# Optimization experiments

Hardware: AMD Instinct MI355X
Metric: run time of the kernel (lower is better)

## Reference

```python
import jax, jax.numpy as jnp
import numpy as np

N = 512      # state dim n
K = 8        # num_regimes
H = 256      # hidden dim for g0/g1/gate MLPs
B = 8192     # batch
INIT_SCALE = 0.1


def _mlp(x, w1, b1, w2, b2, w3, b3):
    # 2 hidden SiLU layers + linear head (matches ScalarMLP/GateNet with num_layers=2)
    h = jax.nn.silu(x @ w1 + b1)
    h = jax.nn.silu(h @ w2 + b2)
    return h @ w3 + b3


def setup_inputs() -> dict:
    key = jax.random.key(0)
    ks = jax.random.split(key, 12)

    def lin(k, fi, fo):
        kw, kb = jax.random.split(k)
        s = 1.0 / np.sqrt(fi)  # torch nn.Linear default init range
        w = jax.random.uniform(kw, (fi, fo), minval=-s, maxval=s, dtype=jnp.float32)
        b = jax.random.uniform(kb, (fo,), minval=-s, maxval=s, dtype=jnp.float32)
        return w, b

    g0_w1, g0_b1 = lin(ks[0], N, H)
    g0_w2, g0_b2 = lin(ks[1], H, H)
    g0_w3, g0_b3 = lin(ks[2], H, 1)
    g1_w1, g1_b1 = lin(ks[3], N, H)
    g1_w2, g1_b2 = lin(ks[4], H, H)
    g1_w3, g1_b3 = lin(ks[5], H, 1)
    gt_w1, gt_b1 = lin(ks[6], N, H)
    gt_w2, gt_b2 = lin(ks[7], H, H)
    gt_w3, gt_b3 = lin(ks[8], H, K)
    W = jax.random.uniform(ks[9], (K, N, N), minval=-INIT_SCALE, maxval=INIT_SCALE, dtype=jnp.float32)
    z = jax.random.normal(ks[10], (B, 2 * N), dtype=jnp.float32)
    return dict(z=z,
                g0_w1=g0_w1, g0_b1=g0_b1, g0_w2=g0_w2, g0_b2=g0_b2, g0_w3=g0_w3, g0_b3=g0_b3,
                g1_w1=g1_w1, g1_b1=g1_b1, g1_w2=g1_w2, g1_b2=g1_b2, g1_w3=g1_w3, g1_b3=g1_b3,
                gt_w1=gt_w1, gt_b1=gt_b1, gt_w2=gt_w2, gt_b2=gt_b2, gt_w3=gt_w3, gt_b3=gt_b3,
                W=W)


def reference(z,
              g0_w1, g0_b1, g0_w2, g0_b2, g0_w3, g0_b3,
              g1_w1, g1_b1, g1_w2, g1_b2, g1_w3, g1_b3,
              gt_w1, gt_b1, gt_w2, gt_b2, gt_w3, gt_b3,
              W):
    n = W.shape[-1]
    x0, x1 = z[:, :n], z[:, n:]

    def U(x0_, x1_):
        e0 = jnp.sum(_mlp(x0_, g0_w1, g0_b1, g0_w2, g0_b2, g0_w3, g0_b3))  # scalar
        e1 = jnp.sum(_mlp(x1_, g1_w1, g1_b1, g1_w2, g1_b2, g1_w3, g1_b3))
        alpha = jax.nn.softmax(_mlp(x0_, gt_w1, gt_b1, gt_w2, gt_b2, gt_w3, gt_b3), axis=-1)  # [B,K]
        # per-sample per-regime bilinear x1^T W_k x0 -> avoids materializing [B,n,n] W_eff
        q = jnp.einsum('bi,kij,bj->bk', x1_, W, x0_)
        return e0 + e1 + jnp.sum(alpha * q)

    grad_x0, grad_x1 = jax.grad(U, argnums=(0, 1))(x0, x1)
    return jnp.concatenate([-grad_x0, -grad_x1], axis=-1)  # [B, 2n]
```

## Files before the change

### kernel.cpp

```cpp
#include <hip/hip_runtime.h>
#include <cstdint>
#include <cstddef>

constexpr int BTOT = 8192, N = 512, H = 256, K = 8;

typedef __attribute__((ext_vector_type(8))) short short8v;
typedef __attribute__((ext_vector_type(4))) float f32x4;

__device__ __forceinline__ float bf2f(unsigned short u) {
    return __uint_as_float(((uint32_t)u) << 16);
}
__device__ __forceinline__ unsigned short f2bf(float f) {
    uint32_t u = __float_as_uint(f);
    uint32_t r = (u + 0x7FFFu + ((u >> 16) & 1u)) >> 16;
    return (unsigned short)r;
}

typedef __attribute__((address_space(3))) unsigned int lds_uint;
typedef __attribute__((address_space(1))) const unsigned int glob_uint;
__device__ __forceinline__ void async16(const unsigned short* g, unsigned short* l) {
    __builtin_amdgcn_global_load_lds((glob_uint*)g, (lds_uint*)l, 16, 0, 0);
}

struct GArg {
    const unsigned short* A;
    const unsigned short* Bt;
    const float* bias;
    const unsigned short* dmul;
    unsigned short* ob;
    unsigned short* ob2;
    float* of;
    int lda, ldbt, Ka, lddm, ldob, ldof;
};
struct GPack { GArg g[5]; };

enum { EPI_BF = 0, EPI_FWD = 1, EPI_BWD2 = 2, EPI_NEG = 3, EPI_NEGW = 4 };

template<int EPI>
__device__ __forceinline__ void gemm_body(const GArg& g, int m0, int n0,
                                          unsigned short* As, unsigned short* Bs)
{
    const int tid = threadIdx.x;
    const int lane = tid & 63, wave = tid >> 6;
    const int wr = (wave >> 1) * 64, wc = (wave & 1) * 64;
    const int rr = lane & 15;
    const int kb = ((lane >> 4) ^ (lane & 3)) << 3;

    const int r0 = tid >> 2;
    const int ko0 = (((tid & 3) ^ (r0 & 3)) << 3);
    const unsigned short* gA0 = g.A + (size_t)(m0 + r0) * g.lda + ko0;
    const unsigned short* gA1 = g.A + (size_t)(m0 + r0 + 64) * g.lda + ko0;
    const unsigned short* gB0 = g.Bt + (size_t)(n0 + r0) * g.ldbt + ko0;
    const unsigned short* gB1 = g.Bt + (size_t)(n0 + r0 + 64) * g.ldbt + ko0;

    auto stage = [&](int t, int buf) {
        const int k0 = t << 5;
        async16(gA0 + k0, As + buf * 4096 + tid * 8);
        async16(gA1 + k0, As + buf * 4096 + (tid + 256) * 8);
        async16(gB0 + k0, Bs + buf * 4096 + tid * 8);
        async16(gB1 + k0, Bs + buf * 4096 + (tid + 256) * 8);
    };

    f32x4 acc[4][4];
    #pragma unroll
    for (int i = 0; i < 4; ++i)
        #pragma unroll
        for (int j = 0; j < 4; ++j) acc[i][j] = (f32x4){0.f, 0.f, 0.f, 0.f};

    const int nt = g.Ka >> 5;

    stage(0, 0);
    if (nt > 1) stage(1, 1);

    int buf = 0;
    for (int t = 0; t < nt; ++t) {
        if (t + 1 < nt) { asm volatile("s_waitcnt vmcnt(4)" ::: "memory"); }
        else            { asm volatile("s_waitcnt vmcnt(0)" ::: "memory"); }
        __builtin_amdgcn_s_barrier();
        if (t + 2 < nt) {
            int b2 = buf + 2; if (b2 >= 3) b2 -= 3;
            stage(t + 2, b2);
        }
        short8v af[4], bfr[4];
        #pragma unroll
        for (int i = 0; i < 4; ++i)
            af[i] = *(const short8v*)(As + buf * 4096 + (wr + i * 16 + rr) * 32 + kb);
        #pragma unroll
        for (int j = 0; j < 4; ++j)
            bfr[j] = *(const short8v*)(Bs + buf * 4096 + (wc + j * 16 + rr) * 32 + kb);
        #pragma unroll
        for (int i = 0; i < 4; ++i)
            #pragma unroll
            for (int j = 0; j < 4; ++j)
                acc[i][j] = __builtin_amdgcn_mfma_f32_16x16x32_bf16(af[i], bfr[j], acc[i][j], 0, 0, 0);
        if (++buf == 3) buf = 0;
    }

    const int orow = (lane >> 4) * 4;
    #pragma unroll
    for (int i = 0; i < 4; ++i) {
        #pragma unroll
        for (int e = 0; e < 4; ++e) {
            const int row = m0 + wr + i * 16 + orow + e;
            #pragma unroll
            for (int j = 0; j < 4; ++j) {
                const int col = n0 + wc + rr + j * 16;
                float v = acc[i][j][e];
                if constexpr (EPI == EPI_BF) {
                    g.ob[(size_t)row * g.ldob + col] = f2bf(v);
                } else if constexpr (EPI == EPI_FWD) {
                    float p = v + g.bias[col];
                    float s = 1.f / (1.f + expf(-p));
                    if (g.ob) g.ob[(size_t)row * g.ldob + col] = f2bf(p * s);
                    g.ob2[(size_t)row * g.ldob + col] = f2bf(s * (1.f + p * (1.f - s)));
                } else if constexpr (EPI == EPI_BWD2) {
                    float t = v * bf2f(g.dmul[(size_t)row * g.lddm + col]);
                    g.ob[(size_t)row * g.ldob + col] = f2bf(t);
                } else if constexpr (EPI == EPI_NEG) {
                    g.of[(size_t)row * g.ldof + col] -= v;
                } else {
                    g.of[(size_t)row * g.ldof + col] = -v;
                }
            }
        }
    }
}

template<int EPI>
__global__ __launch_bounds__(256) void gemm_g(GArg ga0, GArg ga1, GArg ga2)
{
    __shared__ __attribute__((aligned(16))) unsigned short As[3 * 128 * 32];
    __shared__ __attribute__((aligned(16))) unsigned short Bs[3 * 128 * 32];
    const int z = blockIdx.z;
    const GArg g = (z == 0) ? ga0 : (z == 1) ? ga1 : ga2;
    gemm_body<EPI>(g, blockIdx.y * 128, blockIdx.x * 128, As, Bs);
}

__global__ __launch_bounds__(256) void gemm_l1bil(GPack P)
{
    __shared__ __attribute__((aligned(16))) unsigned short As[3 * 128 * 32];
    __shared__ __attribute__((aligned(16))) unsigned short Bs[3 * 128 * 32];
    const int xb = blockIdx.x;
    if (xb < 32) {
        gemm_body<EPI_BF>(P.g[blockIdx.z], blockIdx.y * 128, xb * 128, As, Bs);
    } else {
        gemm_body<EPI_FWD>(P.g[2 + (xb - 32)], blockIdx.y * 128, blockIdx.z * 128, As, Bs);
    }
}

__global__ __launch_bounds__(256) void k_cvt_z(const float* __restrict__ z,
                                               unsigned short* __restrict__ o) {
    int g = (blockIdx.x * 256 + threadIdx.x) * 4;
    float4 v = *(const float4*)(z + g);
    ushort4 u;
    u.x = f2bf(v.x); u.y = f2bf(v.y); u.z = f2bf(v.z); u.w = f2bf(v.w);
    *(ushort4*)(o + g) = u;
}

__global__ __launch_bounds__(256) void k_transpose_w(const float* __restrict__ W,
    unsigned short* __restrict__ Wbf, unsigned short* __restrict__ WTbf)
{
    __shared__ float t[32][33];
    int k = blockIdx.z;
    int i0 = blockIdx.y * 32, j0 = blockIdx.x * 32;
    int tj = threadIdx.x & 31, ti = threadIdx.x >> 5;
    const float* Wk = W + (size_t)k * N * N;
    #pragma unroll
    for (int r = 0; r < 32; r += 8) {
        float v = Wk[(size_t)(i0 + ti + r) * N + j0 + tj];
        t[ti + r][tj] = v;
        Wbf[(size_t)k * N * N + (size_t)(i0 + ti + r) * N + j0 + tj] = f2bf(v);
    }
    __syncthreads();
    #pragma unroll
    for (int r = 0; r < 32; r += 8)
        WTbf[(size_t)k * N * N + (size_t)(j0 + ti + r) * N + i0 + tj] = f2bf(t[tj][ti + r]);
}

struct CvtJob { const float* src; unsigned short* dst; int ls, ld, cols32, tiles, trans; };
struct CvtTable { CvtJob j[12]; };

__global__ __launch_bounds__(256) void k_cvt_w(CvtTable T)
{
    int t = blockIdx.x;
    int ji = 0;
    while (t >= T.j[ji].tiles) { t -= T.j[ji].tiles; ++ji; }
    CvtJob jb = T.j[ji];
    int i0 = (t / jb.cols32) * 32, c0 = (t % jb.cols32) * 32;
    int tc = threadIdx.x & 31, tr = threadIdx.x >> 5;
    if (!jb.trans) {
        #pragma unroll
        for (int r = 0; r < 32; r += 8)
            jb.dst[(size_t)(i0 + tr + r) * jb.ld + c0 + tc] =
                f2bf(jb.src[(size_t)(i0 + tr + r) * jb.ls + c0 + tc]);
    } else {
        __shared__ float tt[32][33];
        #pragma unroll
        for (int r = 0; r < 32; r += 8)
            tt[tr + r][tc] = jb.src[(size_t)(i0 + tr + r) * jb.ls + c0 + tc];
        __syncthreads();
        #pragma unroll
        for (int r = 0; r < 32; r += 8)
            jb.dst[(size_t)(c0 + tr + r) * jb.ld + i0 + tc] = f2bf(tt[tc][tr + r]);
    }
}

__global__ __launch_bounds__(256) void k_head_s(const unsigned short* __restrict__ h2t,
    const float* __restrict__ w3t, const float* __restrict__ b3t,
    float* __restrict__ s)
{
    int t = threadIdx.x;
    int bl = t >> 3, k = t & 7;
    int b = blockIdx.x * 32 + bl;
    const unsigned short* ar = h2t + (size_t)b * H;
    float acc = b3t[k];
    for (int h0 = 0; h0 < H; h0 += 8) {
        short8v hv = *(const short8v*)(ar + h0);
        #pragma unroll
        for (int u = 0; u < 8; ++u)
            acc += bf2f((unsigned short)hv[u]) * w3t[(h0 + u) * K + k];
    }
    s[b * K + k] = acc;
}

__global__ __launch_bounds__(256) void k_q(const unsigned short* __restrict__ v0,
    const unsigned short* __restrict__ zb, float* __restrict__ q)
{
    int w = threadIdx.x >> 6, lane = threadIdx.x & 63;
    int idx = blockIdx.x * 4 + w;
    int b = idx >> 3, k = idx & 7;
    const unsigned short* vr = v0 + ((size_t)b * K + k) * N;
    const unsigned short* xr = zb + (size_t)b * 1024 + 512;
    short8v vv = *(const short8v*)(vr + lane * 8);
    short8v xv = *(const short8v*)(xr + lane * 8);
    float s = 0.f;
    #pragma unroll
    for (int t = 0; t < 8; ++t)
        s += bf2f((unsigned short)vv[t]) * bf2f((unsigned short)xv[t]);
    for (int off = 32; off; off >>= 1) s += __shfl_down(s, off, 64);
    if (lane == 0) q[idx] = s;
}

__global__ __launch_bounds__(256) void k_d(const float* __restrict__ s,
    const float* __restrict__ q, float* __restrict__ alpha,
    float* __restrict__ dd, int Bc)
{
    int b = blockIdx.x * 256 + threadIdx.x;
    if (b >= Bc) return;
    float sv[K], qv[K];
    float m = -1e30f;
    #pragma unroll
    for (int k = 0; k < K; ++k) { sv[k] = s[b * K + k]; m = fmaxf(m, sv[k]); }
    float sum = 0.f;
    #pragma unroll
    for (int k = 0; k < K; ++k) { sv[k] = expf(sv[k] - m); sum += sv[k]; }
    float inv = 1.f / sum, qbar = 0.f;
    #pragma unroll
    for (int k = 0; k < K; ++k) { sv[k] *= inv; qv[k] = q[b * K + k]; qbar += sv[k] * qv[k]; }
    #pragma unroll
    for (int k = 0; k < K; ++k) {
        alpha[b * K + k] = sv[k];
        dd[b * K + k] = sv[k] * (qv[k] - qbar);
    }
}

__global__ __launch_bounds__(256) void k_u2(
    const unsigned short* __restrict__ d2_0, const unsigned short* __restrict__ d2_1,
    const unsigned short* __restrict__ d2_t,
    const float* __restrict__ w3_0, const float* __restrict__ w3_1,
    const float* __restrict__ w3t, const float* __restrict__ dd,
    unsigned short* __restrict__ u2_0, unsigned short* __restrict__ u2_1,
    unsigned short* __restrict__ u2_t)
{
    int g = blockIdx.x * 256 + threadIdx.x;
    int h = g & (H - 1), b = g >> 8;
    u2_0[g] = f2bf(w3_0[h] * bf2f(d2_0[g]));
    u2_1[g] = f2bf(w3_1[h] * bf2f(d2_1[g]));
    float s = 0.f;
    #pragma unroll
    for (int k = 0; k < K; ++k) s += w3t[h * K + k] * dd[b * K + k];
    u2_t[g] = f2bf(s * bf2f(d2_t[g]));
}

__global__ __launch_bounds__(256) void k_gxq2(const unsigned short* __restrict__ v0,
    const unsigned short* __restrict__ v1, const float* __restrict__ alpha,
    float* __restrict__ out)
{
    int g = blockIdx.x * 256 + threadIdx.x;
    int b = g >> 6, jb = (g & 63) << 3;
    float al[K];
    #pragma unroll
    for (int k = 0; k < K; ++k) al[k] = alpha[b * K + k];
    const unsigned short* pv0 = v0 + (size_t)b * K * N + jb;
    const unsigned short* pv1 = v1 + (size_t)b * K * N + jb;
    float s0[8] = {}, s1[8] = {};
    #pragma unroll
    for (int k = 0; k < K; ++k) {
        short8v w1 = *(const short8v*)(pv1 + (size_t)k * N);
        short8v w0 = *(const short8v*)(pv0 + (size_t)k * N);
        #pragma unroll
        for (int t = 0; t < 8; ++t) {
            s0[t] += al[k] * bf2f((unsigned short)w1[t]);
            s1[t] += al[k] * bf2f((unsigned short)w0[t]);
        }
    }
    float* o0 = out + (size_t)b * 1024 + jb;
    float* o1 = o0 + 512;
    float4 x0 = *(float4*)o0, x1 = *(float4*)(o0 + 4);
    x0.x -= s0[0]; x0.y -= s0[1]; x0.z -= s0[2]; x0.w -= s0[3];
    x1.x -= s0[4]; x1.y -= s0[5]; x1.z -= s0[6]; x1.w -= s0[7];
    *(float4*)o0 = x0; *(float4*)(o0 + 4) = x1;
    float4 y0 = *(float4*)o1, y1 = *(float4*)(o1 + 4);
    y0.x -= s1[0]; y0.y -= s1[1]; y0.z -= s1[2]; y0.w -= s1[3];
    y1.x -= s1[4]; y1.y -= s1[5]; y1.z -= s1[6]; y1.w -= s1[7];
    *(float4*)o1 = y0; *(float4*)(o1 + 4) = y1;
}

extern "C" void kernel_launch(void* const* d_in, const int* in_sizes, int n_in,
                              void* d_out, int out_size, void* d_ws, size_t ws_size,
                              hipStream_t stream) {
    const float* z     = (const float*)d_in[0];
    const float* g0_w1 = (const float*)d_in[1];  const float* g0_b1 = (const float*)d_in[2];
    const float* g0_w2 = (const float*)d_in[3];  const float* g0_b2 = (const float*)d_in[4];
    const float* g0_w3 = (const float*)d_in[5];
    const float* g1_w1 = (const float*)d_in[7];  const float* g1_b1 = (const float*)d_in[8];
    const float* g1_w2 = (const float*)d_in[9];  const float* g1_b2 = (const float*)d_in[10];
    const float* g1_w3 = (const float*)d_in[11];
    const float* gt_w1 = (const float*)d_in[13]; const float* gt_b1 = (const float*)d_in[14];
    const float* gt_w2 = (const float*)d_in[15]; const float* gt_b2 = (const float*)d_in[16];
    const float* gt_w3 = (const float*)d_in[17]; const float* gt_b3 = (const float*)d_in[18];
    const float* W     = (const float*)d_in[19];
    float* out = (float*)d_out;

    char* wsb = (char*)d_ws;
    size_t off = 0;
    auto aus = [&](size_t n) -> unsigned short* {
        unsigned short* r = (unsigned short*)(wsb + off);
        off += ((n * 2 + 255) & ~(size_t)255);
        return r;
    };
    auto af4 = [&](size_t n) -> float* {
        float* r = (float*)(wsb + off);
        off += ((n * 4 + 255) & ~(size_t)255);
        return r;
    };

    unsigned short* Zbf  = aus((size_t)BTOT * 1024);
    unsigned short* Wbf  = aus((size_t)K * N * N);
    unsigned short* WTbf = aus((size_t)K * N * N);
    unsigned short* w1T[3], *w2T[3], *w2N[3];
    for (int i = 0; i < 3; ++i) w1T[i] = aus((size_t)H * N);
    for (int i = 0; i < 3; ++i) w2T[i] = aus((size_t)H * H);
    for (int i = 0; i < 3; ++i) w2N[i] = aus((size_t)H * H);
    unsigned short* w1N1  = aus((size_t)N * H);
    unsigned short* w1cat = aus((size_t)N * 2 * H);
    unsigned short* h1[3], *d1b[3], *d2b[3], *u2[3];
    for (int i = 0; i < 3; ++i) h1[i]  = aus((size_t)BTOT * H);
    for (int i = 0; i < 3; ++i) d1b[i] = aus((size_t)BTOT * H);
    for (int i = 0; i < 3; ++i) d2b[i] = aus((size_t)BTOT * H);
    for (int i = 0; i < 3; ++i) u2[i]  = aus((size_t)BTOT * H);
    unsigned short* h2t   = aus((size_t)BTOT * H);
    unsigned short* t2cat = aus((size_t)BTOT * 512);
    unsigned short* t21   = aus((size_t)BTOT * H);
    float* sbuf = af4((size_t)BTOT * K);
    float* qbuf = af4((size_t)BTOT * K);
    float* abuf = af4((size_t)BTOT * K);
    float* dbuf = af4((size_t)BTOT * K);

    int Bcv = BTOT;
    while (off + 2 * (((size_t)Bcv * K * N * 2 + 255) & ~(size_t)255) > ws_size && Bcv > 128)
        Bcv >>= 1;
    unsigned short* v0 = aus((size_t)Bcv * K * N);
    unsigned short* v1 = aus((size_t)Bcv * K * N);
    const bool full = (Bcv == BTOT);

    const dim3 blk(256);

    if (!full)
        hipMemsetAsync(d_out, 0, (size_t)out_size * sizeof(float), stream);

    k_cvt_z<<<BTOT * 1024 / (256 * 4), blk, 0, stream>>>(z, Zbf);
    k_transpose_w<<<dim3(N / 32, N / 32, K), blk, 0, stream>>>(W, Wbf, WTbf);

    CvtTable T;
    int nj = 0, tot = 0;
    auto addjob = [&](const float* src, int ls, unsigned short* dst, int ld,
                      int rows, int cols, int trans) {
        CvtJob jb; jb.src = src; jb.dst = dst; jb.ls = ls; jb.ld = ld;
        jb.cols32 = cols / 32; jb.tiles = (rows / 32) * (cols / 32); jb.trans = trans;
        T.j[nj++] = jb; tot += jb.tiles;
    };
    addjob(g0_w1, H, w1T[0], N, N, H, 1);
    addjob(g1_w1, H, w1T[1], N, N, H, 1);
    addjob(gt_w1, H, w1T[2], N, N, H, 1);
    addjob(g0_w2, H, w2T[0], H, H, H, 1);
    addjob(g1_w2, H, w2T[1], H, H, H, 1);
    addjob(gt_w2, H, w2T[2], H, H, H, 1);
    addjob(g0_w2, H, w2N[0], H, H, H, 0);
    addjob(g1_w2, H, w2N[1], H, H, H, 0);
    addjob(gt_w2, H, w2N[2], H, H, H, 0);
    addjob(g1_w1, H, w1N1, H, N, H, 0);
    addjob(g0_w1, H, w1cat, 2 * H, N, H, 0);
    addjob(gt_w1, H, w1cat + H, 2 * H, N, H, 0);
    k_cvt_w<<<tot, blk, 0, stream>>>(T);

    auto mk = [](const unsigned short* A, int lda, const unsigned short* Bt, int ldbt, int Ka) {
        GArg g; g.A = A; g.Bt = Bt; g.bias = nullptr; g.dmul = nullptr;
        g.ob = nullptr; g.ob2 = nullptr; g.of = nullptr;
        g.lda = lda; g.ldbt = ldbt; g.Ka = Ka; g.lddm = 0; g.ldob = 0; g.ldof = 0;
        return g;
    };

    const float* bs1[3] = {g0_b1, g1_b1, gt_b1};

    if (full) {
        GPack P;
        P.g[0] = mk(Zbf, 1024, Wbf, N, N);
        P.g[0].ob = v0; P.g[0].ldob = K * N;
        P.g[1] = mk(Zbf + 512, 1024, WTbf, N, N);
        P.g[1].ob = v1; P.g[1].ldob = K * N;
        for (int i = 0; i < 3; ++i) {
            P.g[2 + i] = mk(Zbf + (i == 1 ? 512 : 0), 1024, w1T[i], N, N);
            P.g[2 + i].bias = bs1[i]; P.g[2 + i].ob = h1[i];
            P.g[2 + i].ob2 = d1b[i];  P.g[2 + i].ldob = H;
        }
        gemm_l1bil<<<dim3(35, BTOT / 128, 2), blk, 0, stream>>>(P);
    } else {
        GArg a[3];
        for (int i = 0; i < 3; ++i) {
            a[i] = mk(Zbf + (i == 1 ? 512 : 0), 1024, w1T[i], N, N);
            a[i].bias = bs1[i]; a[i].ob = h1[i]; a[i].ob2 = d1b[i]; a[i].ldob = H;
        }
        gemm_g<EPI_FWD><<<dim3(H / 128, BTOT / 128, 3), blk, 0, stream>>>(a[0], a[1], a[2]);
    }

    {
        const float* bs[3] = {g0_b2, g1_b2, gt_b2};
        GArg a[3];
        for (int i = 0; i < 3; ++i) {
            a[i] = mk(h1[i], H, w2T[i], H, H);
            a[i].bias = bs[i]; a[i].ob = (i == 2) ? h2t : nullptr;
            a[i].ob2 = d2b[i]; a[i].ldob = H;
        }
        gemm_g<EPI_FWD><<<dim3(H / 128, BTOT / 128, 3), blk, 0, stream>>>(a[0], a[1], a[2]);
    }
    k_head_s<<<BTOT / 32, blk, 0, stream>>>(h2t, gt_w3, gt_b3, sbuf);

    for (int cb = 0; cb < BTOT; cb += Bcv) {
        if (!full) {
            GArg a[2];
            a[0] = mk(Zbf + (size_t)cb * 1024, 1024, Wbf, N, N);
            a[0].ob = v0; a[0].ldob = K * N;
            a[1] = mk(Zbf + (size_t)cb * 1024 + 512, 1024, WTbf, N, N);
            a[1].ob = v1; a[1].ldob = K * N;
            gemm_g<EPI_BF><<<dim3(K * N / 128, Bcv / 128, 2), blk, 0, stream>>>(a[0], a[1], a[1]);
        }
        k_q<<<Bcv * K / 4, blk, 0, stream>>>(v0, Zbf + (size_t)cb * 1024, qbuf + (size_t)cb * K);
        k_d<<<(Bcv + 255) / 256, blk, 0, stream>>>(sbuf + (size_t)cb * K, qbuf + (size_t)cb * K,
                                                   abuf + (size_t)cb * K, dbuf + (size_t)cb * K, Bcv);
        if (!full)
            k_gxq2<<<Bcv * 64 / 256, blk, 0, stream>>>(v0, v1, abuf + (size_t)cb * K,
                                                       out + (size_t)cb * 1024);
    }

    k_u2<<<BTOT * H / 256, blk, 0, stream>>>(d2b[0], d2b[1], d2b[2],
                                             g0_w3, g1_w3, gt_w3, dbuf,
                                             u2[0], u2[1], u2[2]);

    {
        GArg a[3];
        a[0] = mk(u2[0], H, w2N[0], H, H);
        a[0].dmul = d1b[0]; a[0].lddm = H; a[0].ob = t2cat;     a[0].ldob = 512;
        a[1] = mk(u2[1], H, w2N[1], H, H);
        a[1].dmul = d1b[1]; a[1].lddm = H; a[1].ob = t21;       a[1].ldob = H;
        a[2] = mk(u2[2], H, w2N[2], H, H);
        a[2].dmul = d1b[2]; a[2].lddm = H; a[2].ob = t2cat + H; a[2].ldob = 512;
        gemm_g<EPI_BWD2><<<dim3(H / 128, BTOT / 128, 3), blk, 0, stream>>>(a[0], a[1], a[2]);
    }
    {
        GArg a[2];
        a[0] = mk(t2cat, 512, w1cat, 2 * H, 512);
        a[0].of = out;       a[0].ldof = 1024;
        a[1] = mk(t21, H, w1N1, H, H);
        a[1].of = out + 512; a[1].ldof = 1024;
        if (full) {
            gemm_g<EPI_NEGW><<<dim3(N / 128, BTOT / 128, 2), blk, 0, stream>>>(a[0], a[1], a[1]);
            k_gxq2<<<BTOT * 64 / 256, blk, 0, stream>>>(v0, v1, abuf, out);
        } else {
            gemm_g<EPI_NEG><<<dim3(N / 128, BTOT / 128, 2), blk, 0, stream>>>(a[0], a[1], a[1]);
        }
    }
}
```

Before: 265.3 us.

## Fuse bilinear q reduction into v0 GEMM epilogue and w3 scaling into layer-2 epilogue

The layer-2 forward epilogue now multiplies the SiLU derivative by w3 for the two scalar MLPs and writes u2 directly. This removes the d2 intermediates and most of the k_u2 elementwise pass. In the full path, the fused layer-1/bilinear kernel is split back into separate launches. The v0 GEMM epilogue now loads the matching x1 tile into LDS and computes per-row partial dot products, accumulated into q with atomics, so k_q no longer runs. The trade-offs are atomic contention, a zeroing memset, extra LDS traffic in the epilogue, and the loss of the combined layer-1/bilinear launch.

New measurement: 276.4 us. 4.2% more time.

```diff
diff --git a/kernel.cpp b/kernel.cpp
--- a/kernel.cpp
+++ b/kernel.cpp
@@ -26,22 +26,29 @@
     const unsigned short* A;
     const unsigned short* Bt;
     const float* bias;
+    const float* w3v;
     const unsigned short* dmul;
     unsigned short* ob;
     unsigned short* ob2;
     float* of;
+    float* qout;
+    const unsigned short* xq;
     int lda, ldbt, Ka, lddm, ldob, ldof;
 };
-struct GPack { GArg g[5]; };
 
 enum { EPI_BF = 0, EPI_FWD = 1, EPI_BWD2 = 2, EPI_NEG = 3, EPI_NEGW = 4 };
 
 template<int EPI>
-__device__ __forceinline__ void gemm_body(const GArg& g, int m0, int n0,
-                                          unsigned short* As, unsigned short* Bs)
-{
+__global__ __launch_bounds__(256) void gemm_g(GArg ga0, GArg ga1, GArg ga2)
+{
+    const int z = blockIdx.z;
+    const GArg g = (z == 0) ? ga0 : (z == 1) ? ga1 : ga2;
+
+    __shared__ __attribute__((aligned(16))) unsigned short As[3 * 128 * 32];
+    __shared__ __attribute__((aligned(16))) unsigned short Bs[3 * 128 * 32];
     const int tid = threadIdx.x;
     const int lane = tid & 63, wave = tid >> 6;
+    const int m0 = blockIdx.y * 128, n0 = blockIdx.x * 128;
     const int wr = (wave >> 1) * 64, wc = (wave & 1) * 64;
     const int rr = lane & 15;
     const int kb = ((lane >> 4) ^ (lane & 3)) << 3;
@@ -112,7 +119,9 @@
                     float p = v + g.bias[col];
                     float s = 1.f / (1.f + expf(-p));
                     if (g.ob) g.ob[(size_t)row * g.ldob + col] = f2bf(p * s);
-                    g.ob2[(size_t)row * g.ldob + col] = f2bf(s * (1.f + p * (1.f - s)));
+                    float ds = s * (1.f + p * (1.f - s));
+                    if (g.w3v) ds *= g.w3v[col];
+                    g.ob2[(size_t)row * g.ldob + col] = f2bf(ds);
                 } else if constexpr (EPI == EPI_BWD2) {
                     float t = v * bf2f(g.dmul[(size_t)row * g.lddm + col]);
                     g.ob[(size_t)row * g.ldob + col] = f2bf(t);
@@ -124,27 +133,40 @@
             }
         }
     }
-}
-
-template<int EPI>
-__global__ __launch_bounds__(256) void gemm_g(GArg ga0, GArg ga1, GArg ga2)
-{
-    __shared__ __attribute__((aligned(16))) unsigned short As[3 * 128 * 32];
-    __shared__ __attribute__((aligned(16))) unsigned short Bs[3 * 128 * 32];
-    const int z = blockIdx.z;
-    const GArg g = (z == 0) ? ga0 : (z == 1) ? ga1 : ga2;
-    gemm_body<EPI>(g, blockIdx.y * 128, blockIdx.x * 128, As, Bs);
-}
-
-__global__ __launch_bounds__(256) void gemm_l1bil(GPack P)
-{
-    __shared__ __attribute__((aligned(16))) unsigned short As[3 * 128 * 32];
-    __shared__ __attribute__((aligned(16))) unsigned short Bs[3 * 128 * 32];
-    const int xb = blockIdx.x;
-    if (xb < 32) {
-        gemm_body<EPI_BF>(P.g[blockIdx.z], blockIdx.y * 128, xb * 128, As, Bs);
-    } else {
-        gemm_body<EPI_FWD>(P.g[2 + (xb - 32)], blockIdx.y * 128, blockIdx.z * 128, As, Bs);
+
+    if constexpr (EPI == EPI_BF) {
+        if (g.qout) {
+            const int kq = n0 >> 9, i0 = n0 & 511;
+            __syncthreads();
+            #pragma unroll
+            for (int it = 0; it < 8; ++it) {
+                int ci = tid + it * 256;
+                int rg = ci >> 4, co = (ci & 15) << 3;
+                const unsigned short* src = g.xq + (size_t)(m0 + rg) * 1024 + i0 + co;
+                unsigned short* dst = (it < 4 ? As : Bs) + (rg & 63) * 128 + co;
+                async16(src, dst);
+            }
+            asm volatile("s_waitcnt vmcnt(0)" ::: "memory");
+            __builtin_amdgcn_s_barrier();
+            const unsigned short* half = (wr == 0) ? As : Bs;
+            #pragma unroll
+            for (int i = 0; i < 4; ++i) {
+                #pragma unroll
+                for (int e = 0; e < 4; ++e) {
+                    const int rl = i * 16 + orow + e;
+                    float sq = 0.f;
+                    #pragma unroll
+                    for (int j = 0; j < 4; ++j)
+                        sq += acc[i][j][e] * bf2f(half[rl * 128 + wc + rr + j * 16]);
+                    sq += __shfl_xor(sq, 1, 64);
+                    sq += __shfl_xor(sq, 2, 64);
+                    sq += __shfl_xor(sq, 4, 64);
+                    sq += __shfl_xor(sq, 8, 64);
+                    if (rr == 0)
+                        atomicAdd(g.qout + (size_t)(m0 + wr + rl) * K + kq, sq);
+                }
+            }
+        }
     }
 }
 
@@ -264,18 +286,13 @@
     }
 }
 
-__global__ __launch_bounds__(256) void k_u2(
-    const unsigned short* __restrict__ d2_0, const unsigned short* __restrict__ d2_1,
+__global__ __launch_bounds__(256) void k_u2t(
     const unsigned short* __restrict__ d2_t,
-    const float* __restrict__ w3_0, const float* __restrict__ w3_1,
     const float* __restrict__ w3t, const float* __restrict__ dd,
-    unsigned short* __restrict__ u2_0, unsigned short* __restrict__ u2_1,
     unsigned short* __restrict__ u2_t)
 {
     int g = blockIdx.x * 256 + threadIdx.x;
     int h = g & (H - 1), b = g >> 8;
-    u2_0[g] = f2bf(w3_0[h] * bf2f(d2_0[g]));
-    u2_1[g] = f2bf(w3_1[h] * bf2f(d2_1[g]));
     float s = 0.f;
     #pragma unroll
     for (int k = 0; k < K; ++k) s += w3t[h * K + k] * dd[b * K + k];
@@ -354,11 +371,11 @@
     for (int i = 0; i < 3; ++i) w2N[i] = aus((size_t)H * H);
     unsigned short* w1N1  = aus((size_t)N * H);
     unsigned short* w1cat = aus((size_t)N * 2 * H);
-    unsigned short* h1[3], *d1b[3], *d2b[3], *u2[3];
+    unsigned short* h1[3], *d1b[3], *u2[3];
     for (int i = 0; i < 3; ++i) h1[i]  = aus((size_t)BTOT * H);
     for (int i = 0; i < 3; ++i) d1b[i] = aus((size_t)BTOT * H);
-    for (int i = 0; i < 3; ++i) d2b[i] = aus((size_t)BTOT * H);
     for (int i = 0; i < 3; ++i) u2[i]  = aus((size_t)BTOT * H);
+    unsigned short* d2t   = aus((size_t)BTOT * H);
     unsigned short* h2t   = aus((size_t)BTOT * H);
     unsigned short* t2cat = aus((size_t)BTOT * 512);
     unsigned short* t21   = aus((size_t)BTOT * H);
@@ -378,6 +395,8 @@
 
     if (!full)
         hipMemsetAsync(d_out, 0, (size_t)out_size * sizeof(float), stream);
+    if (full)
+        hipMemsetAsync(qbuf, 0, (size_t)BTOT * K * sizeof(float), stream);
 
     k_cvt_z<<<BTOT * 1024 / (256 * 4), blk, 0, stream>>>(z, Zbf);
     k_transpose_w<<<dim3(N / 32, N / 32, K), blk, 0, stream>>>(W, Wbf, WTbf);
@@ -405,57 +424,52 @@
     k_cvt_w<<<tot, blk, 0, stream>>>(T);
 
     auto mk = [](const unsigned short* A, int lda, const unsigned short* Bt, int ldbt, int Ka) {
-        GArg g; g.A = A; g.Bt = Bt; g.bias = nullptr; g.dmul = nullptr;
+        GArg g; g.A = A; g.Bt = Bt; g.bias = nullptr; g.w3v = nullptr; g.dmul = nullptr;
         g.ob = nullptr; g.ob2 = nullptr; g.of = nullptr;
+        g.qout = nullptr; g.xq = nullptr;
         g.lda = lda; g.ldbt = ldbt; g.Ka = Ka; g.lddm = 0; g.ldob = 0; g.ldof = 0;
         return g;
     };
 
-    const float* bs1[3] = {g0_b1, g1_b1, gt_b1};
-
-    if (full) {
-        GPack P;
-        P.g[0] = mk(Zbf, 1024, Wbf, N, N);
-        P.g[0].ob = v0; P.g[0].ldob = K * N;
-        P.g[1] = mk(Zbf + 512, 1024, WTbf, N, N);
-        P.g[1].ob = v1; P.g[1].ldob = K * N;
-        for (int i = 0; i < 3; ++i) {
-            P.g[2 + i] = mk(Zbf + (i == 1 ? 512 : 0), 1024, w1T[i], N, N);
-            P.g[2 + i].bias = bs1[i]; P.g[2 + i].ob = h1[i];
-            P.g[2 + i].ob2 = d1b[i];  P.g[2 + i].ldob = H;
-        }
-        gemm_l1bil<<<dim3(35, BTOT / 128, 2), blk, 0, stream>>>(P);
-    } else {
+    {
+        const float* bs[3] = {g0_b1, g1_b1, gt_b1};
         GArg a[3];
         for (int i = 0; i < 3; ++i) {
             a[i] = mk(Zbf + (i == 1 ? 512 : 0), 1024, w1T[i], N, N);
-            a[i].bias = bs1[i]; a[i].ob = h1[i]; a[i].ob2 = d1b[i]; a[i].ldob = H;
+            a[i].bias = bs[i]; a[i].ob = h1[i]; a[i].ob2 = d1b[i]; a[i].ldob = H;
         }
         gemm_g<EPI_FWD><<<dim3(H / 128, BTOT / 128, 3), blk, 0, stream>>>(a[0], a[1], a[2]);
     }
-
     {
         const float* bs[3] = {g0_b2, g1_b2, gt_b2};
+        const float* w3[3] = {g0_w3, g1_w3, nullptr};
         GArg a[3];
         for (int i = 0; i < 3; ++i) {
             a[i] = mk(h1[i], H, w2T[i], H, H);
-            a[i].bias = bs[i]; a[i].ob = (i == 2) ? h2t : nullptr;
-            a[i].ob2 = d2b[i]; a[i].ldob = H;
+            a[i].bias = bs[i];
+            a[i].w3v = w3[i];
+            a[i].ob  = (i == 2) ? h2t : nullptr;
+            a[i].ob2 = (i == 2) ? d2t : u2[i];
+            a[i].ldob = H;
         }
         gemm_g<EPI_FWD><<<dim3(H / 128, BTOT / 128, 3), blk, 0, stream>>>(a[0], a[1], a[2]);
     }
     k_head_s<<<BTOT / 32, blk, 0, stream>>>(h2t, gt_w3, gt_b3, sbuf);
 
     for (int cb = 0; cb < BTOT; cb += Bcv) {
-        if (!full) {
-            GArg a[2];
-            a[0] = mk(Zbf + (size_t)cb * 1024, 1024, Wbf, N, N);
-            a[0].ob = v0; a[0].ldob = K * N;
-            a[1] = mk(Zbf + (size_t)cb * 1024 + 512, 1024, WTbf, N, N);
-            a[1].ob = v1; a[1].ldob = K * N;
-            gemm_g<EPI_BF><<<dim3(K * N / 128, Bcv / 128, 2), blk, 0, stream>>>(a[0], a[1], a[1]);
-        }
-        k_q<<<Bcv * K / 4, blk, 0, stream>>>(v0, Zbf + (size_t)cb * 1024, qbuf + (size_t)cb * K);
+        GArg a[2];
+        a[0] = mk(Zbf + (size_t)cb * 1024, 1024, Wbf, N, N);
+        a[0].ob = v0; a[0].ldob = K * N;
+        if (full) {
+            a[0].qout = qbuf;
+            a[0].xq = Zbf + 512;
+        }
+        a[1] = mk(Zbf + (size_t)cb * 1024 + 512, 1024, WTbf, N, N);
+        a[1].ob = v1; a[1].ldob = K * N;
+        gemm_g<EPI_BF><<<dim3(K * N / 128, Bcv / 128, 2), blk, 0, stream>>>(a[0], a[1], a[1]);
+
+        if (!full)
+            k_q<<<Bcv * K / 4, blk, 0, stream>>>(v0, Zbf + (size_t)cb * 1024, qbuf + (size_t)cb * K);
         k_d<<<(Bcv + 255) / 256, blk, 0, stream>>>(sbuf + (size_t)cb * K, qbuf + (size_t)cb * K,
                                                    abuf + (size_t)cb * K, dbuf + (size_t)cb * K, Bcv);
         if (!full)
@@ -463,9 +477,7 @@
                                                        out + (size_t)cb * 1024);
     }
 
-    k_u2<<<BTOT * H / 256, blk, 0, stream>>>(d2b[0], d2b[1], d2b[2],
-                                             g0_w3, g1_w3, gt_w3, dbuf,
-                                             u2[0], u2[1], u2[2]);
+    k_u2t<<<BTOT * H / 256, blk, 0, stream>>>(d2t, gt_w3, dbuf, u2[2]);
 
     {
         GArg a[3];
```
